# Optimization experiments

Measured on AMD Instinct MI355X. Metric: run time of the kernel, lower is better.

Reference implementation:

```python
import jax, jax.numpy as jnp
import numpy as np

N1, F_IN, E1 = 50000, 128, 1000000   # data1: 10 graphs x 5000 nodes
B, NPG = 10, 5000
N2, E2 = 199, 4000                    # data2: fixed by fc1 in-dim 9950 = 50*199
K = 50
LN_EPS = 1e-5


def setup_inputs() -> dict:
    key = jax.random.key(0)
    ks = jax.random.split(key, 24)
    s = lambda k, shape: (jax.random.normal(k, shape, jnp.float32) * 0.05)
    inp = {}
    inp["x1"] = jax.random.normal(ks[0], (N1, F_IN), jnp.float32)
    inp["edge_index1"] = jax.random.randint(ks[1], (2, E1), 0, N1, jnp.int32)
    inp["batch1"] = jnp.repeat(jnp.arange(B, dtype=jnp.int32), NPG)  # equal-size graphs
    inp["x2"] = jax.random.normal(ks[2], (N2, F_IN), jnp.float32)
    inp["edge_index2"] = jax.random.randint(ks[3], (2, E2), 0, N2, jnp.int32)
    # GNN params (shared Siamese weights). PyG SAGEConv: lin_l (aggr, has bias), lin_r (root, no bias)
    inp["w1l"] = s(ks[4], (128, F_IN)); inp["b1l"] = jnp.zeros((128,), jnp.float32)
    inp["w1r"] = s(ks[5], (128, F_IN))
    inp["w2l"] = s(ks[6], (64, 128));   inp["b2l"] = jnp.zeros((64,), jnp.float32)
    inp["w2r"] = s(ks[7], (64, 128))
    # MLP head
    inp["fc1_w"] = s(ks[8], (128, K * N2)); inp["fc1_b"] = jnp.zeros((128,), jnp.float32)
    inp["ln1_g"] = jnp.ones((128,), jnp.float32); inp["ln1_b"] = jnp.zeros((128,), jnp.float32)
    inp["fc2_w"] = s(ks[9], (64, 128)); inp["fc2_b"] = jnp.zeros((64,), jnp.float32)
    inp["ln2_g"] = jnp.ones((64,), jnp.float32); inp["ln2_b"] = jnp.zeros((64,), jnp.float32)
    inp["fc3_w"] = s(ks[10], (1, 64)); inp["fc3_b"] = jnp.zeros((1,), jnp.float32)
    return inp


def _sage(x, edge_index, wl, bl, wr, n_nodes):
    # mean aggregation of source features at target nodes, then two linears
    src, dst = edge_index[0], edge_index[1]
    msg_sum = jax.ops.segment_sum(x[src], dst, num_segments=n_nodes)
    cnt = jax.ops.segment_sum(jnp.ones((edge_index.shape[1], 1), x.dtype), dst,
                              num_segments=n_nodes)
    mean = msg_sum / jnp.maximum(cnt, 1.0)
    return mean @ wl.T + bl + x @ wr.T


def _gnn(x, ei, w1l, b1l, w1r, w2l, b2l, w2r):
    n = x.shape[0]
    h = jax.nn.relu(_sage(x, ei, w1l, b1l, w1r, n))
    return jax.nn.relu(_sage(h, ei, w2l, b2l, w2r, n))


def _layernorm(x, g, b):
    mu = jnp.mean(x, -1, keepdims=True)
    var = jnp.mean((x - mu) ** 2, -1, keepdims=True)
    return (x - mu) * jax.lax.rsqrt(var + LN_EPS) * g + b


def reference(x1, edge_index1, batch1, x2, edge_index2,
              w1l, b1l, w1r, w2l, b2l, w2r,
              fc1_w, fc1_b, ln1_g, ln1_b, fc2_w, fc2_b, ln2_g, ln2_b, fc3_w, fc3_b):
    out1 = _gnn(x1, edge_index1, w1l, b1l, w1r, w2l, b2l, w2r)   # [N1, 64]
    out2 = _gnn(x2, edge_index2, w1l, b1l, w1r, w2l, b2l, w2r)   # [N2, 64]
    # cdist p=2
    a2 = jnp.sum(out1 * out1, -1, keepdims=True)                 # [N1,1]
    b2 = jnp.sum(out2 * out2, -1)                                # [N2]
    d2 = a2 + b2[None, :] - 2.0 * (out1 @ out2.T)
    dist = jnp.sqrt(jnp.maximum(d2, 0.0))                        # [N1, N2]
    # SortAggregation(k=50): per-graph sort rows by last column (desc), take top k.
    # batch1 groups equal-size graphs contiguously -> reshape is exact dense batching.
    xb = dist.reshape(B, NPG, N2)
    order = jnp.argsort(-xb[:, :, -1], axis=1)[:, :K]            # [B, K]
    topk = jnp.take_along_axis(xb, order[:, :, None], axis=1)    # [B, K, N2]
    out = topk.reshape(B, K * N2)
    out = jax.nn.relu(_layernorm(out @ fc1_w.T + fc1_b, ln1_g, ln1_b))
    out = jax.nn.relu(_layernorm(out @ fc2_w.T + fc2_b, ln2_g, ln2_b))
    out = jax.nn.sigmoid(out @ fc3_w.T + fc3_b)                  # [B, 1]
    return out
```

## Files before the change

kernel.cpp:

```cpp
#include <hip/hip_runtime.h>
#include <math.h>

#define N1 50000
#define F_IN 128
#define E1 1000000
#define Bg 10
#define NPG 5000
#define N2 199
#define E2 4000
#define KSEL 50
#define LN_EPS 1e-5f
#define CHUNKS 8
#define CHSZ 625
#define EBT 8192
#define NB 49
#define BCAP 24576

typedef unsigned long long ull;

__global__ void k_bucket(const int* __restrict__ ei1, int* __restrict__ bcnt,
                         unsigned int* __restrict__ bed,
                         const int* __restrict__ ei2, int* __restrict__ rp2,
                         int* __restrict__ srcs2) {
  int t = threadIdx.x;
  int blk = blockIdx.x;
  const int nEdgeBlocks = (E1 + EBT - 1) / EBT;
  if (blk == nEdgeBlocks) {
    __shared__ int cnt2[N2];
    __shared__ int cur2[N2];
    const int* src = ei2;
    const int* dst = ei2 + E2;
    for (int i = t; i < N2; i += 256) cnt2[i] = 0;
    __syncthreads();
    for (int e = t; e < E2; e += 256) atomicAdd(&cnt2[dst[e]], 1);
    __syncthreads();
    if (t == 0) {
      int run = 0;
      rp2[0] = 0;
      for (int i = 0; i < N2; i++) {
        cur2[i] = run;
        run += cnt2[i];
        rp2[i + 1] = run;
      }
    }
    __syncthreads();
    for (int e = t; e < E2; e += 256) {
      int d = dst[e];
      int pos = atomicAdd(&cur2[d], 1);
      srcs2[pos] = src[e];
    }
    return;
  }
  __shared__ int hcnt[NB];
  const int* src = ei1;
  const int* dst = ei1 + E1;
  int e0 = blk * EBT;
  int e1 = min(e0 + EBT, E1);
  if (t < NB) hcnt[t] = 0;
  __syncthreads();
  for (int e = e0 + t; e < e1; e += 256) atomicAdd(&hcnt[dst[e] >> 10], 1);
  __syncthreads();
  if (t < NB) hcnt[t] = atomicAdd(&bcnt[t], hcnt[t]);
  __syncthreads();
  for (int e = e0 + t; e < e1; e += 256) {
    int d = dst[e];
    int s = src[e];
    int b = d >> 10;
    int pos = atomicAdd(&hcnt[b], 1);
    if (pos < BCAP)
      bed[(size_t)b * BCAP + pos] = ((unsigned int)(d & 1023) << 16) | (unsigned int)s;
  }
}

__global__ __launch_bounds__(1024) void k_csr_bucket(
    const int* __restrict__ bcnt, const unsigned int* __restrict__ bed,
    int* __restrict__ rp, int* __restrict__ srcs) {
  __shared__ int cnt[1024];
  __shared__ int cur[1024];
  __shared__ int wsums[16];
  __shared__ int s_bbase;
  int b = blockIdx.x, t = threadIdx.x;
  int lane = t & 63, w = t >> 6;
  int total = bcnt[b];
  if (total > BCAP) total = BCAP;
  cnt[t] = 0;
  if (w == 0) {
    int vb = (lane < b) ? min(bcnt[lane], BCAP) : 0;
    for (int off = 32; off; off >>= 1) vb += __shfl_xor(vb, off);
    if (lane == 0) s_bbase = vb;
  }
  __syncthreads();
  const unsigned int* list = bed + (size_t)b * BCAP;
  for (int e = t; e < total; e += 1024) atomicAdd(&cnt[list[e] >> 16], 1);
  __syncthreads();
  int v = cnt[t];
  int x = v;
#pragma unroll
  for (int off = 1; off < 64; off <<= 1) {
    int y = __shfl_up(x, off);
    if (lane >= off) x += y;
  }
  if (lane == 63) wsums[w] = x;
  __syncthreads();
  if (w == 0) {
    int s = (lane < 16) ? wsums[lane] : 0;
#pragma unroll
    for (int off = 1; off < 16; off <<= 1) {
      int y = __shfl_up(s, off);
      if (lane >= off) s += y;
    }
    if (lane < 16) wsums[lane] = s;
  }
  __syncthreads();
  int incl = x + (w > 0 ? wsums[w - 1] : 0);
  int bbase = s_bbase;
  int node = b * 1024 + t;
  if (node < N1) rp[node + 1] = bbase + incl;
  cur[t] = bbase + incl - v;
  if (b == 0 && t == 0) rp[0] = 0;
  __syncthreads();
  for (int e = t; e < total; e += 1024) {
    unsigned int pe = list[e];
    int dl = pe >> 16;
    int pos = atomicAdd(&cur[dl], 1);
    srcs[pos] = (int)(pe & 0xFFFFu);
  }
}

__global__ void k_aggr128(const float* __restrict__ xA, const int* __restrict__ rpA,
                          const int* __restrict__ srcsA, float* __restrict__ meanA, int nA,
                          const float* __restrict__ xB, const int* __restrict__ rpB,
                          const int* __restrict__ srcsB, float* __restrict__ meanB, int nB,
                          int blocksA) {
  int blk = blockIdx.x;
  const float* x;
  const int* rp;
  const int* srcs;
  float* mean;
  int n, nb0;
  if (blk < blocksA) { x = xA; rp = rpA; srcs = srcsA; mean = meanA; n = nA; nb0 = blk * 4; }
  else { x = xB; rp = rpB; srcs = srcsB; mean = meanB; n = nB; nb0 = (blk - blocksA) * 4; }
  int lane = threadIdx.x & 63;
  int node = nb0 + (threadIdx.x >> 6);
  if (node >= n) return;
  int s = rp[node], e = rp[node + 1];
  const float2* xp = (const float2*)x;
  float2 acc = make_float2(0.f, 0.f);
  int i = s;
  for (; i + 8 <= e; i += 8) {
    int s0 = srcs[i], s1 = srcs[i + 1], s2 = srcs[i + 2], s3 = srcs[i + 3];
    int s4 = srcs[i + 4], s5 = srcs[i + 5], s6 = srcs[i + 6], s7 = srcs[i + 7];
    float2 v0 = xp[(size_t)s0 * 64 + lane];
    float2 v1 = xp[(size_t)s1 * 64 + lane];
    float2 v2 = xp[(size_t)s2 * 64 + lane];
    float2 v3 = xp[(size_t)s3 * 64 + lane];
    float2 v4 = xp[(size_t)s4 * 64 + lane];
    float2 v5 = xp[(size_t)s5 * 64 + lane];
    float2 v6 = xp[(size_t)s6 * 64 + lane];
    float2 v7 = xp[(size_t)s7 * 64 + lane];
    acc.x += ((v0.x + v1.x) + (v2.x + v3.x)) + ((v4.x + v5.x) + (v6.x + v7.x));
    acc.y += ((v0.y + v1.y) + (v2.y + v3.y)) + ((v4.y + v5.y) + (v6.y + v7.y));
  }
  for (; i < e; i++) {
    float2 v = xp[(size_t)srcs[i] * 64 + lane];
    acc.x += v.x;
    acc.y += v.y;
  }
  float c = (float)((e - s) > 0 ? (e - s) : 1);
  float2 o = make_float2(acc.x / c, acc.y / c);
  *(float2*)&mean[(size_t)node * 128 + lane * 2] = o;
}

__global__ void k_aggr_fused64(const float* __restrict__ zA, const int* __restrict__ rpA,
                               const int* __restrict__ srcsA, float* __restrict__ outA, int nA,
                               const float* __restrict__ zB, const int* __restrict__ rpB,
                               const int* __restrict__ srcsB, float* __restrict__ outB, int nB,
                               const float* __restrict__ bias, int blocksA) {
  int blk = blockIdx.x;
  const float* zlr;
  const int* rp;
  const int* srcs;
  float* out;
  int n, nb0;
  if (blk < blocksA) { zlr = zA; rp = rpA; srcs = srcsA; out = outA; n = nA; nb0 = blk * 4; }
  else { zlr = zB; rp = rpB; srcs = srcsB; out = outB; n = nB; nb0 = (blk - blocksA) * 4; }
  int lane = threadIdx.x & 63;
  int node = nb0 + (threadIdx.x >> 6);
  if (node >= n) return;
  int s = rp[node], e = rp[node + 1];
  float acc = 0.f;
  int i = s;
  for (; i + 8 <= e; i += 8) {
    int s0 = srcs[i], s1 = srcs[i + 1], s2 = srcs[i + 2], s3 = srcs[i + 3];
    int s4 = srcs[i + 4], s5 = srcs[i + 5], s6 = srcs[i + 6], s7 = srcs[i + 7];
    float v0 = zlr[(size_t)s0 * 128 + lane];
    float v1 = zlr[(size_t)s1 * 128 + lane];
    float v2 = zlr[(size_t)s2 * 128 + lane];
    float v3 = zlr[(size_t)s3 * 128 + lane];
    float v4 = zlr[(size_t)s4 * 128 + lane];
    float v5 = zlr[(size_t)s5 * 128 + lane];
    float v6 = zlr[(size_t)s6 * 128 + lane];
    float v7 = zlr[(size_t)s7 * 128 + lane];
    acc += ((v0 + v1) + (v2 + v3)) + ((v4 + v5) + (v6 + v7));
  }
  for (; i < e; i++) acc += zlr[(size_t)srcs[i] * 128 + lane];
  float c = (float)((e - s) > 0 ? (e - s) : 1);
  float v = acc / c + bias[lane] + zlr[(size_t)node * 128 + 64 + lane];
  out[(size_t)node * 64 + lane] = v > 0.f ? v : 0.f;
}

__global__ __launch_bounds__(256) void k_sage_gemm128(
    const float* __restrict__ xinA, const float* __restrict__ meanA,
    float* __restrict__ outA, int nA,
    const float* __restrict__ xinB, const float* __restrict__ meanB,
    float* __restrict__ outB, int nB,
    const float* __restrict__ wl, const float* __restrict__ bl,
    const float* __restrict__ wr, int blocksA) {
  constexpr int TM = 128, TK = 32;
  constexpr int SA = TM + 4;
  constexpr int SW = 128 + 4;
  __shared__ float s_a[TK][SA];
  __shared__ float s_w[TK][SW];
  int blk = blockIdx.x;
  const float* xin;
  const float* mean;
  float* out;
  int n, m0;
  if (blk < blocksA) { xin = xinA; mean = meanA; out = outA; n = nA; m0 = blk * TM; }
  else { xin = xinB; mean = meanB; out = outB; n = nB; m0 = (blk - blocksA) * TM; }
  int t = threadIdx.x;
  int tx = t & 15, ty = t >> 4;
  int sub = t >> 3;
  int kv = (t & 7) << 2;

  float acc[8][8];
#pragma unroll
  for (int i = 0; i < 8; i++)
#pragma unroll
    for (int j = 0; j < 8; j++) acc[i][j] = 0.f;

  for (int ph = 0; ph < 2; ph++) {
    const float* A = ph ? xin : mean;
    const float* W = ph ? wr : wl;
    for (int k0 = 0; k0 < 128; k0 += TK) {
      __syncthreads();
#pragma unroll
      for (int p = 0; p < 4; p++) {
        int node = m0 + p * 32 + sub;
        float4 v = make_float4(0.f, 0.f, 0.f, 0.f);
        if (node < n) v = *(const float4*)&A[(size_t)node * 128 + k0 + kv];
        int col = p * 32 + sub;
        s_a[kv + 0][col] = v.x;
        s_a[kv + 1][col] = v.y;
        s_a[kv + 2][col] = v.z;
        s_a[kv + 3][col] = v.w;
      }
#pragma unroll
      for (int p = 0; p < 4; p++) {
        int j = p * 32 + sub;
        float4 v = *(const float4*)&W[(size_t)j * 128 + k0 + kv];
        s_w[kv + 0][j] = v.x;
        s_w[kv + 1][j] = v.y;
        s_w[kv + 2][j] = v.z;
        s_w[kv + 3][j] = v.w;
      }
      __syncthreads();
#pragma unroll 8
      for (int kk = 0; kk < TK; kk++) {
        float4 a0 = *(const float4*)&s_a[kk][ty * 8];
        float4 a1 = *(const float4*)&s_a[kk][ty * 8 + 4];
        float av[8] = {a0.x, a0.y, a0.z, a0.w, a1.x, a1.y, a1.z, a1.w};
        float4 w0 = *(const float4*)&s_w[kk][tx * 8];
        float4 w1 = *(const float4*)&s_w[kk][tx * 8 + 4];
        float wv[8] = {w0.x, w0.y, w0.z, w0.w, w1.x, w1.y, w1.z, w1.w};
#pragma unroll
        for (int i = 0; i < 8; i++)
#pragma unroll
          for (int j = 0; j < 8; j++) acc[i][j] = fmaf(av[i], wv[j], acc[i][j]);
      }
    }
  }
  float bj[8];
#pragma unroll
  for (int j = 0; j < 8; j++) bj[j] = bl[tx * 8 + j];
#pragma unroll
  for (int i = 0; i < 8; i++) {
    int node = m0 + ty * 8 + i;
    if (node < n) {
#pragma unroll
      for (int q = 0; q < 8; q += 4) {
        float v0 = acc[i][q + 0] + bj[q + 0];
        float v1 = acc[i][q + 1] + bj[q + 1];
        float v2 = acc[i][q + 2] + bj[q + 2];
        float v3 = acc[i][q + 3] + bj[q + 3];
        float4 o;
        o.x = v0 > 0.f ? v0 : 0.f;
        o.y = v1 > 0.f ? v1 : 0.f;
        o.z = v2 > 0.f ? v2 : 0.f;
        o.w = v3 > 0.f ? v3 : 0.f;
        *(float4*)&out[(size_t)node * 128 + tx * 8 + q] = o;
      }
    }
  }
}

__global__ __launch_bounds__(256) void k_lin_dual(
    const float* __restrict__ AA, float* __restrict__ zA, int nA,
    const float* __restrict__ AB, float* __restrict__ zB, int nB,
    const float* __restrict__ wl, const float* __restrict__ wr, int blocksA) {
  constexpr int TM = 128, TK = 32;
  constexpr int SA = TM + 4;
  constexpr int SW = 128 + 4;
  __shared__ float s_a[TK][SA];
  __shared__ float s_w[TK][SW];
  int blk = blockIdx.x;
  const float* A;
  float* zlr;
  int n, m0;
  if (blk < blocksA) { A = AA; zlr = zA; n = nA; m0 = blk * TM; }
  else { A = AB; zlr = zB; n = nB; m0 = (blk - blocksA) * TM; }
  int t = threadIdx.x;
  int tx = t & 15, ty = t >> 4;
  int sub = t >> 3;
  int kv = (t & 7) << 2;

  float acc[8][8];
#pragma unroll
  for (int i = 0; i < 8; i++)
#pragma unroll
    for (int j = 0; j < 8; j++) acc[i][j] = 0.f;

  for (int k0 = 0; k0 < 128; k0 += TK) {
    __syncthreads();
#pragma unroll
    for (int p = 0; p < 4; p++) {
      int node = m0 + p * 32 + sub;
      float4 v = make_float4(0.f, 0.f, 0.f, 0.f);
      if (node < n) v = *(const float4*)&A[(size_t)node * 128 + k0 + kv];
      int col = p * 32 + sub;
      s_a[kv + 0][col] = v.x;
      s_a[kv + 1][col] = v.y;
      s_a[kv + 2][col] = v.z;
      s_a[kv + 3][col] = v.w;
    }
#pragma unroll
    for (int p = 0; p < 4; p++) {
      int j = p * 32 + sub;
      const float* W = (j < 64) ? &wl[(size_t)j * 128] : &wr[(size_t)(j - 64) * 128];
      float4 v = *(const float4*)&W[k0 + kv];
      s_w[kv + 0][j] = v.x;
      s_w[kv + 1][j] = v.y;
      s_w[kv + 2][j] = v.z;
      s_w[kv + 3][j] = v.w;
    }
    __syncthreads();
#pragma unroll 8
    for (int kk = 0; kk < TK; kk++) {
      float4 a0 = *(const float4*)&s_a[kk][ty * 8];
      float4 a1 = *(const float4*)&s_a[kk][ty * 8 + 4];
      float av[8] = {a0.x, a0.y, a0.z, a0.w, a1.x, a1.y, a1.z, a1.w};
      float4 w0 = *(const float4*)&s_w[kk][tx * 8];
      float4 w1 = *(const float4*)&s_w[kk][tx * 8 + 4];
      float wv[8] = {w0.x, w0.y, w0.z, w0.w, w1.x, w1.y, w1.z, w1.w};
#pragma unroll
      for (int i = 0; i < 8; i++)
#pragma unroll
        for (int j = 0; j < 8; j++) acc[i][j] = fmaf(av[i], wv[j], acc[i][j]);
    }
  }
#pragma unroll
  for (int i = 0; i < 8; i++) {
    int node = m0 + ty * 8 + i;
    if (node < n) {
#pragma unroll
      for (int q = 0; q < 8; q += 4) {
        float4 o = make_float4(acc[i][q + 0], acc[i][q + 1], acc[i][q + 2], acc[i][q + 3]);
        *(float4*)&zlr[(size_t)node * 128 + tx * 8 + q] = o;
      }
    }
  }
}

__global__ void k_score_topk_local(const float* __restrict__ out1,
                                   const float* __restrict__ out2,
                                   ull* __restrict__ cand) {
  __shared__ ull s[1024];
  __shared__ float brow[64];
  int blk = blockIdx.x;
  int b = blk >> 3, c = blk & 7;
  int t = threadIdx.x;
  if (t < 64) brow[t] = out2[198 * 64 + t];
  __syncthreads();
  const float4* b4 = (const float4*)brow;
  float b2 = 0.f;
#pragma unroll
  for (int q = 0; q < 16; q++) {
    float4 w = b4[q];
    b2 = fmaf(w.x, w.x, fmaf(w.y, w.y, fmaf(w.z, w.z, fmaf(w.w, w.w, b2))));
  }
#pragma unroll
  for (int p = 0; p < 4; p++) {
    int i = p * 256 + t;
    ull key = 0ULL;
    if (i < CHSZ) {
      int gidx = c * CHSZ + i;
      const float4* ap = (const float4*)&out1[((size_t)b * NPG + gidx) * 64];
      float dot = 0.f, a2 = 0.f;
#pragma unroll
      for (int q = 0; q < 16; q++) {
        float4 a = ap[q];
        float4 w = b4[q];
        dot = fmaf(a.x, w.x, fmaf(a.y, w.y, fmaf(a.z, w.z, fmaf(a.w, w.w, dot))));
        a2 = fmaf(a.x, a.x, fmaf(a.y, a.y, fmaf(a.z, a.z, fmaf(a.w, a.w, a2))));
      }
      float d2 = a2 + b2 - 2.f * dot;
      float sc = sqrtf(fmaxf(d2, 0.f));
      key = ((ull)__float_as_uint(sc) << 32) | (unsigned int)(~gidx);
    }
    s[i] = key;
  }
  __syncthreads();
  for (int k = 2; k <= 1024; k <<= 1) {
    for (int j = k >> 1; j > 0; j >>= 1) {
#pragma unroll
      for (int p = 0; p < 4; p++) {
        int i = p * 256 + t;
        int l = i ^ j;
        if (l > i) {
          bool up = ((i & k) != 0);
          ull a = s[i], bb = s[l];
          if ((a > bb) == up) { s[i] = bb; s[l] = a; }
        }
      }
      __syncthreads();
    }
  }
  if (t < KSEL) cand[(b * CHUNKS + c) * KSEL + t] = s[t];
}

__global__ void k_topk_merge(const ull* __restrict__ cand, int* __restrict__ sel) {
  __shared__ ull s[512];
  int b = blockIdx.x, t = threadIdx.x;
#pragma unroll
  for (int p = 0; p < 2; p++) {
    int i = p * 256 + t;
    s[i] = (i < CHUNKS * KSEL) ? cand[b * CHUNKS * KSEL + i] : 0ULL;
  }
  __syncthreads();
  for (int k = 2; k <= 512; k <<= 1) {
    for (int j = k >> 1; j > 0; j >>= 1) {
#pragma unroll
      for (int p = 0; p < 2; p++) {
        int i = p * 256 + t;
        int l = i ^ j;
        if (l > i) {
          bool up = ((i & k) != 0);
          ull a = s[i], bb = s[l];
          if ((a > bb) == up) { s[i] = bb; s[l] = a; }
        }
      }
      __syncthreads();
    }
  }
  if (t < KSEL) {
    int gidx = (int)(~((unsigned int)s[t]));
    sel[b * KSEL + t] = b * NPG + gidx;
  }
}

__global__ void k_dist_rows(const float* __restrict__ out1, const float* __restrict__ out2,
                            const int* __restrict__ sel, float* __restrict__ D) {
  __shared__ float arow[64];
  int i = blockIdx.x;
  int t = threadIdx.x;
  int node = sel[i];
  if (t < 64) arow[t] = out1[(size_t)node * 64 + t];
  __syncthreads();
  float a2 = 0.f;
#pragma unroll
  for (int f = 0; f < 64; f++) a2 = fmaf(arow[f], arow[f], a2);
  for (int nn = t; nn < N2; nn += 256) {
    float dot = 0.f, b2 = 0.f;
#pragma unroll 8
    for (int f = 0; f < 64; f++) {
      float bv = out2[nn * 64 + f];
      dot = fmaf(arow[f], bv, dot);
      b2 = fmaf(bv, bv, b2);
    }
    float d2 = a2 + b2 - 2.f * dot;
    D[i * N2 + nn] = sqrtf(fmaxf(d2, 0.f));
  }
}

__global__ void k_fc1_dot(const float* __restrict__ D, const float* __restrict__ w,
                          float* __restrict__ h1pre) {
  constexpr int M = KSEL * N2;
  constexpr int M2 = M / 2;
  int b = blockIdx.x >> 7;
  int j = blockIdx.x & 127;
  int t = threadIdx.x;
  const float2* wp = (const float2*)(w + (size_t)j * M);
  const float2* dp = (const float2*)(D + (size_t)b * M);
  float acc = 0.f;
  for (int m = t; m < M2; m += 256) {
    float2 wv = wp[m];
    float2 dv = dp[m];
    acc = fmaf(dv.x, wv.x, acc);
    acc = fmaf(dv.y, wv.y, acc);
  }
  for (int off = 32; off; off >>= 1) acc += __shfl_xor(acc, off);
  __shared__ float ws_[4];
  int lane = t & 63, wv_ = t >> 6;
  if (lane == 0) ws_[wv_] = acc;
  __syncthreads();
  if (t == 0) h1pre[b * 128 + j] = ws_[0] + ws_[1] + ws_[2] + ws_[3];
}

__global__ void k_fc123(const float* __restrict__ h1pre, const float* __restrict__ fc1b,
                        const float* __restrict__ g1, const float* __restrict__ be1,
                        const float* __restrict__ w2, const float* __restrict__ b2v,
                        const float* __restrict__ g2, const float* __restrict__ be2,
                        const float* __restrict__ w3, const float* __restrict__ b3,
                        float* __restrict__ out) {
  __shared__ float wsum[2];
  __shared__ float sh[128];
  int b = blockIdx.x, t = threadIdx.x;
  float acc = h1pre[b * 128 + t] + fc1b[t];
  int lane = t & 63, wv_ = t >> 6;
  float ssum = acc;
  for (int off = 32; off; off >>= 1) ssum += __shfl_xor(ssum, off);
  if (lane == 0) wsum[wv_] = ssum;
  __syncthreads();
  float mu = (wsum[0] + wsum[1]) / 128.f;
  __syncthreads();
  float d = acc - mu;
  float vv = d * d;
  for (int off = 32; off; off >>= 1) vv += __shfl_xor(vv, off);
  if (lane == 0) wsum[wv_] = vv;
  __syncthreads();
  float var = (wsum[0] + wsum[1]) / 128.f;
  float r = rsqrtf(var + LN_EPS);
  float h = d * r * g1[t] + be1[t];
  sh[t] = h > 0.f ? h : 0.f;
  __syncthreads();
  if (t < 64) {
    float a2 = b2v[t];
#pragma unroll 8
    for (int k = 0; k < 128; k++) a2 = fmaf(sh[k], w2[t * 128 + k], a2);
    float s2 = a2;
    for (int off = 32; off; off >>= 1) s2 += __shfl_xor(s2, off);
    float mu2 = s2 * (1.f / 64.f);
    float d2 = a2 - mu2;
    float vv2 = d2 * d2;
    for (int off = 32; off; off >>= 1) vv2 += __shfl_xor(vv2, off);
    float r2 = rsqrtf(vv2 * (1.f / 64.f) + LN_EPS);
    float h2 = d2 * r2 * g2[t] + be2[t];
    h2 = h2 > 0.f ? h2 : 0.f;
    float pp = h2 * w3[t];
    for (int off = 32; off; off >>= 1) pp += __shfl_xor(pp, off);
    if (t == 0) out[b] = 1.f / (1.f + expf(-(pp + b3[0])));
  }
}

extern "C" void kernel_launch(void* const* d_in, const int* in_sizes, int n_in,
                              void* d_out, int out_size, void* d_ws, size_t ws_size,
                              hipStream_t stream) {
  const float* x1 = (const float*)d_in[0];
  const int* ei1 = (const int*)d_in[1];
  const float* x2 = (const float*)d_in[3];
  const int* ei2 = (const int*)d_in[4];
  const float* w1l = (const float*)d_in[5];
  const float* b1l = (const float*)d_in[6];
  const float* w1r = (const float*)d_in[7];
  const float* w2l = (const float*)d_in[8];
  const float* b2l = (const float*)d_in[9];
  const float* w2r = (const float*)d_in[10];
  const float* fc1w = (const float*)d_in[11];
  const float* fc1b = (const float*)d_in[12];
  const float* ln1g = (const float*)d_in[13];
  const float* ln1b = (const float*)d_in[14];
  const float* fc2w = (const float*)d_in[15];
  const float* fc2b = (const float*)d_in[16];
  const float* ln2g = (const float*)d_in[17];
  const float* ln2b = (const float*)d_in[18];
  const float* fc3w = (const float*)d_in[19];
  const float* fc3b = (const float*)d_in[20];
  float* out = (float*)d_out;

  char* p = (char*)d_ws;
  auto alloc = [&](size_t bytes) {
    char* r = p;
    p += (bytes + 255) & ~(size_t)255;
    return r;
  };
  int* rp1 = (int*)alloc((N1 + 1) * 4);
  int* bcnt = (int*)alloc(NB * 4);
  unsigned int* bed = (unsigned int*)alloc((size_t)NB * BCAP * 4);
  int* srcs1 = (int*)alloc((size_t)E1 * 4);
  int* rp2 = (int*)alloc((N2 + 1) * 4);
  int* srcs2 = (int*)alloc(E2 * 4);
  float* bufMean = (float*)alloc((size_t)N1 * 128 * 4);
  float* bufH = (float*)alloc((size_t)N1 * 128 * 4);
  float* out1b = (float*)alloc((size_t)N1 * 64 * 4);
  float* mean2 = (float*)alloc((size_t)N2 * 128 * 4);
  float* h2g = (float*)alloc((size_t)N2 * 128 * 4);
  float* out2b = (float*)alloc((size_t)N2 * 64 * 4);
  int* sel = (int*)alloc(Bg * KSEL * 4);
  ull* cand = (ull*)alloc((size_t)Bg * CHUNKS * KSEL * 8);
  float* Dm = (float*)alloc((size_t)Bg * KSEL * N2 * 4);
  float* h1pre = (float*)alloc(Bg * 128 * 4);

  const int nEdgeBlocks = (E1 + EBT - 1) / EBT;
  const int aggrBlocksA = (N1 + 3) / 4;
  const int aggrBlocksB = (N2 + 3) / 4;
  const int gemmBlocksA = (N1 + 127) / 128;
  const int gemmBlocksB = (N2 + 127) / 128;

  hipMemsetAsync(bcnt, 0, NB * 4, stream);
  k_bucket<<<nEdgeBlocks + 1, 256, 0, stream>>>(ei1, bcnt, bed, ei2, rp2, srcs2);
  k_csr_bucket<<<NB, 1024, 0, stream>>>(bcnt, bed, rp1, srcs1);
  k_aggr128<<<aggrBlocksA + aggrBlocksB, 256, 0, stream>>>(
      x1, rp1, srcs1, bufMean, N1, x2, rp2, srcs2, mean2, N2, aggrBlocksA);
  k_sage_gemm128<<<gemmBlocksA + gemmBlocksB, 256, 0, stream>>>(
      x1, bufMean, bufH, N1, x2, mean2, h2g, N2, w1l, b1l, w1r, gemmBlocksA);
  k_lin_dual<<<gemmBlocksA + gemmBlocksB, 256, 0, stream>>>(
      bufH, bufMean, N1, h2g, mean2, N2, w2l, w2r, gemmBlocksA);
  k_aggr_fused64<<<aggrBlocksA + aggrBlocksB, 256, 0, stream>>>(
      bufMean, rp1, srcs1, out1b, N1, mean2, rp2, srcs2, out2b, N2, b2l, aggrBlocksA);
  k_score_topk_local<<<Bg * CHUNKS, 256, 0, stream>>>(out1b, out2b, cand);
  k_topk_merge<<<Bg, 256, 0, stream>>>(cand, sel);
  k_dist_rows<<<Bg * KSEL, 256, 0, stream>>>(out1b, out2b, sel, Dm);
  k_fc1_dot<<<Bg * 128, 256, 0, stream>>>(Dm, fc1w, h1pre);
  k_fc123<<<Bg, 128, 0, stream>>>(h1pre, fc1b, ln1g, ln1b, fc2w, fc2b, ln2g, ln2b,
                                  fc3w, fc3b, out);
}
```

Measured before the change: 415.0 us.

## Fuse SAGE layer-1 and layer-2 GEMMs, merge topk with dist, batch fc1

Merges the layer-1 SAGE GEMM and the layer-2 dual linear into one kernel with 64-row tiles. The intermediate hidden activations stay in shared memory (transposed) instead of round-tripping through a global buffer. It also fuses the top-k merge with the distance-row computation, dropping one launch and the sel buffer. The fc1 dot is restructured so each block handles one output column for all 10 graphs, so fc1 weights are read once instead of ten times. The trade-offs are larger shared memory per block, smaller M-tiles, fewer blocks in the merge/dist and fc1 stages, and an in-place overwrite of bufMean that depends on each block reading only its own rows.

```diff
diff --git a/kernel.cpp b/kernel.cpp
--- a/kernel.cpp
+++ b/kernel.cpp
@@ -209,173 +209,127 @@
   out[(size_t)node * 64 + lane] = v > 0.f ? v : 0.f;
 }
 
-__global__ __launch_bounds__(256) void k_sage_gemm128(
-    const float* __restrict__ xinA, const float* __restrict__ meanA,
-    float* __restrict__ outA, int nA,
-    const float* __restrict__ xinB, const float* __restrict__ meanB,
-    float* __restrict__ outB, int nB,
-    const float* __restrict__ wl, const float* __restrict__ bl,
-    const float* __restrict__ wr, int blocksA) {
-  constexpr int TM = 128, TK = 32;
-  constexpr int SA = TM + 4;
-  constexpr int SW = 128 + 4;
-  __shared__ float s_a[TK][SA];
-  __shared__ float s_w[TK][SW];
+__global__ __launch_bounds__(256) void k_sage12(
+    const float* __restrict__ xinA, float* __restrict__ zA, int nA,
+    const float* __restrict__ xinB, float* __restrict__ zB, int nB,
+    const float* __restrict__ w1l, const float* __restrict__ b1l,
+    const float* __restrict__ w1r, const float* __restrict__ w2l,
+    const float* __restrict__ w2r, int blocksA) {
+  constexpr int TM = 64, TK = 32;
+  __shared__ float s_a[TK][TM + 4];
+  __shared__ float s_w[TK][132];
+  __shared__ float s_hT[128][TM + 4];
   int blk = blockIdx.x;
   const float* xin;
-  const float* mean;
-  float* out;
+  float* zlr;
   int n, m0;
-  if (blk < blocksA) { xin = xinA; mean = meanA; out = outA; n = nA; m0 = blk * TM; }
-  else { xin = xinB; mean = meanB; out = outB; n = nB; m0 = (blk - blocksA) * TM; }
+  if (blk < blocksA) { xin = xinA; zlr = zA; n = nA; m0 = blk * TM; }
+  else { xin = xinB; zlr = zB; n = nB; m0 = (blk - blocksA) * TM; }
   int t = threadIdx.x;
   int tx = t & 15, ty = t >> 4;
-  int sub = t >> 3;
-  int kv = (t & 7) << 2;
-
-  float acc[8][8];
-#pragma unroll
-  for (int i = 0; i < 8; i++)
+
+  float acc[4][8];
+#pragma unroll
+  for (int i = 0; i < 4; i++)
 #pragma unroll
     for (int j = 0; j < 8; j++) acc[i][j] = 0.f;
 
   for (int ph = 0; ph < 2; ph++) {
-    const float* A = ph ? xin : mean;
-    const float* W = ph ? wr : wl;
+    const float* A = ph ? xin : zlr;
+    const float* W = ph ? w1r : w1l;
     for (int k0 = 0; k0 < 128; k0 += TK) {
       __syncthreads();
 #pragma unroll
+      for (int p = 0; p < 2; p++) {
+        int idx = p * 256 + t;
+        int nl = idx >> 3, kq = (idx & 7) << 2;
+        int gn = m0 + nl;
+        float4 v = make_float4(0.f, 0.f, 0.f, 0.f);
+        if (gn < n) v = *(const float4*)&A[(size_t)gn * 128 + k0 + kq];
+        s_a[kq + 0][nl] = v.x;
+        s_a[kq + 1][nl] = v.y;
+        s_a[kq + 2][nl] = v.z;
+        s_a[kq + 3][nl] = v.w;
+      }
+#pragma unroll
       for (int p = 0; p < 4; p++) {
-        int node = m0 + p * 32 + sub;
-        float4 v = make_float4(0.f, 0.f, 0.f, 0.f);
-        if (node < n) v = *(const float4*)&A[(size_t)node * 128 + k0 + kv];
-        int col = p * 32 + sub;
-        s_a[kv + 0][col] = v.x;
-        s_a[kv + 1][col] = v.y;
-        s_a[kv + 2][col] = v.z;
-        s_a[kv + 3][col] = v.w;
-      }
-#pragma unroll
-      for (int p = 0; p < 4; p++) {
-        int j = p * 32 + sub;
-        float4 v = *(const float4*)&W[(size_t)j * 128 + k0 + kv];
-        s_w[kv + 0][j] = v.x;
-        s_w[kv + 1][j] = v.y;
-        s_w[kv + 2][j] = v.z;
-        s_w[kv + 3][j] = v.w;
+        int idx = p * 256 + t;
+        int j = idx >> 3, kq = (idx & 7) << 2;
+        float4 v = *(const float4*)&W[(size_t)j * 128 + k0 + kq];
+        s_w[kq + 0][j] = v.x;
+        s_w[kq + 1][j] = v.y;
+        s_w[kq + 2][j] = v.z;
+        s_w[kq + 3][j] = v.w;
       }
       __syncthreads();
 #pragma unroll 8
       for (int kk = 0; kk < TK; kk++) {
-        float4 a0 = *(const float4*)&s_a[kk][ty * 8];
-        float4 a1 = *(const float4*)&s_a[kk][ty * 8 + 4];
-        float av[8] = {a0.x, a0.y, a0.z, a0.w, a1.x, a1.y, a1.z, a1.w};
+        float4 a0 = *(const float4*)&s_a[kk][ty * 4];
+        float av[4] = {a0.x, a0.y, a0.z, a0.w};
         float4 w0 = *(const float4*)&s_w[kk][tx * 8];
         float4 w1 = *(const float4*)&s_w[kk][tx * 8 + 4];
         float wv[8] = {w0.x, w0.y, w0.z, w0.w, w1.x, w1.y, w1.z, w1.w};
 #pragma unroll
-        for (int i = 0; i < 8; i++)
+        for (int i = 0; i < 4; i++)
 #pragma unroll
           for (int j = 0; j < 8; j++) acc[i][j] = fmaf(av[i], wv[j], acc[i][j]);
       }
     }
   }
-  float bj[8];
-#pragma unroll
-  for (int j = 0; j < 8; j++) bj[j] = bl[tx * 8 + j];
-#pragma unroll
-  for (int i = 0; i < 8; i++) {
-    int node = m0 + ty * 8 + i;
-    if (node < n) {
-#pragma unroll
-      for (int q = 0; q < 8; q += 4) {
-        float v0 = acc[i][q + 0] + bj[q + 0];
-        float v1 = acc[i][q + 1] + bj[q + 1];
-        float v2 = acc[i][q + 2] + bj[q + 2];
-        float v3 = acc[i][q + 3] + bj[q + 3];
-        float4 o;
-        o.x = v0 > 0.f ? v0 : 0.f;
-        o.y = v1 > 0.f ? v1 : 0.f;
-        o.z = v2 > 0.f ? v2 : 0.f;
-        o.w = v3 > 0.f ? v3 : 0.f;
-        *(float4*)&out[(size_t)node * 128 + tx * 8 + q] = o;
-      }
-    }
-  }
-}
-
-__global__ __launch_bounds__(256) void k_lin_dual(
-    const float* __restrict__ AA, float* __restrict__ zA, int nA,
-    const float* __restrict__ AB, float* __restrict__ zB, int nB,
-    const float* __restrict__ wl, const float* __restrict__ wr, int blocksA) {
-  constexpr int TM = 128, TK = 32;
-  constexpr int SA = TM + 4;
-  constexpr int SW = 128 + 4;
-  __shared__ float s_a[TK][SA];
-  __shared__ float s_w[TK][SW];
-  int blk = blockIdx.x;
-  const float* A;
-  float* zlr;
-  int n, m0;
-  if (blk < blocksA) { A = AA; zlr = zA; n = nA; m0 = blk * TM; }
-  else { A = AB; zlr = zB; n = nB; m0 = (blk - blocksA) * TM; }
-  int t = threadIdx.x;
-  int tx = t & 15, ty = t >> 4;
-  int sub = t >> 3;
-  int kv = (t & 7) << 2;
-
-  float acc[8][8];
-#pragma unroll
-  for (int i = 0; i < 8; i++)
-#pragma unroll
-    for (int j = 0; j < 8; j++) acc[i][j] = 0.f;
-
+  __syncthreads();
+#pragma unroll
+  for (int q = 0; q < 8; q++) {
+    int j = tx * 8 + q;
+    float b = b1l[j];
+    float4 hv;
+    float h0 = acc[0][q] + b, h1 = acc[1][q] + b, h2 = acc[2][q] + b, h3 = acc[3][q] + b;
+    hv.x = h0 > 0.f ? h0 : 0.f;
+    hv.y = h1 > 0.f ? h1 : 0.f;
+    hv.z = h2 > 0.f ? h2 : 0.f;
+    hv.w = h3 > 0.f ? h3 : 0.f;
+    *(float4*)&s_hT[j][ty * 4] = hv;
+  }
+
+  float acc2[4][8];
+#pragma unroll
+  for (int i = 0; i < 4; i++)
+#pragma unroll
+    for (int j = 0; j < 8; j++) acc2[i][j] = 0.f;
   for (int k0 = 0; k0 < 128; k0 += TK) {
     __syncthreads();
 #pragma unroll
     for (int p = 0; p < 4; p++) {
-      int node = m0 + p * 32 + sub;
-      float4 v = make_float4(0.f, 0.f, 0.f, 0.f);
-      if (node < n) v = *(const float4*)&A[(size_t)node * 128 + k0 + kv];
-      int col = p * 32 + sub;
-      s_a[kv + 0][col] = v.x;
-      s_a[kv + 1][col] = v.y;
-      s_a[kv + 2][col] = v.z;
-      s_a[kv + 3][col] = v.w;
-    }
-#pragma unroll
-    for (int p = 0; p < 4; p++) {
-      int j = p * 32 + sub;
-      const float* W = (j < 64) ? &wl[(size_t)j * 128] : &wr[(size_t)(j - 64) * 128];
-      float4 v = *(const float4*)&W[k0 + kv];
-      s_w[kv + 0][j] = v.x;
-      s_w[kv + 1][j] = v.y;
-      s_w[kv + 2][j] = v.z;
-      s_w[kv + 3][j] = v.w;
+      int idx = p * 256 + t;
+      int j = idx >> 3, kq = (idx & 7) << 2;
+      const float* W2 = (j < 64) ? &w2l[(size_t)j * 128] : &w2r[(size_t)(j - 64) * 128];
+      float4 v = *(const float4*)&W2[k0 + kq];
+      s_w[kq + 0][j] = v.x;
+      s_w[kq + 1][j] = v.y;
+      s_w[kq + 2][j] = v.z;
+      s_w[kq + 3][j] = v.w;
     }
     __syncthreads();
 #pragma unroll 8
     for (int kk = 0; kk < TK; kk++) {
-      float4 a0 = *(const float4*)&s_a[kk][ty * 8];
-      float4 a1 = *(const float4*)&s_a[kk][ty * 8 + 4];
-      float av[8] = {a0.x, a0.y, a0.z, a0.w, a1.x, a1.y, a1.z, a1.w};
+      float4 a0 = *(const float4*)&s_hT[k0 + kk][ty * 4];
+      float av[4] = {a0.x, a0.y, a0.z, a0.w};
       float4 w0 = *(const float4*)&s_w[kk][tx * 8];
       float4 w1 = *(const float4*)&s_w[kk][tx * 8 + 4];
       float wv[8] = {w0.x, w0.y, w0.z, w0.w, w1.x, w1.y, w1.z, w1.w};
 #pragma unroll
-      for (int i = 0; i < 8; i++)
-#pragma unroll
-        for (int j = 0; j < 8; j++) acc[i][j] = fmaf(av[i], wv[j], acc[i][j]);
-    }
-  }
-#pragma unroll
-  for (int i = 0; i < 8; i++) {
-    int node = m0 + ty * 8 + i;
-    if (node < n) {
+      for (int i = 0; i < 4; i++)
+#pragma unroll
+        for (int j = 0; j < 8; j++) acc2[i][j] = fmaf(av[i], wv[j], acc2[i][j]);
+    }
+  }
+#pragma unroll
+  for (int i = 0; i < 4; i++) {
+    int gn = m0 + ty * 4 + i;
+    if (gn < n) {
 #pragma unroll
       for (int q = 0; q < 8; q += 4) {
-        float4 o = make_float4(acc[i][q + 0], acc[i][q + 1], acc[i][q + 2], acc[i][q + 3]);
-        *(float4*)&zlr[(size_t)node * 128 + tx * 8 + q] = o;
+        float4 o = make_float4(acc2[i][q + 0], acc2[i][q + 1], acc2[i][q + 2], acc2[i][q + 3]);
+        *(float4*)&zlr[(size_t)gn * 128 + tx * 8 + q] = o;
       }
     }
   }
@@ -438,8 +392,12 @@
   if (t < KSEL) cand[(b * CHUNKS + c) * KSEL + t] = s[t];
 }
 
-__global__ void k_topk_merge(const ull* __restrict__ cand, int* __restrict__ sel) {
+__global__ void k_merge_dist(const ull* __restrict__ cand, const float* __restrict__ out1,
+                             const float* __restrict__ out2, float* __restrict__ D) {
   __shared__ ull s[512];
+  __shared__ float s_a[KSEL][64];
+  __shared__ float s_a2[KSEL];
+  __shared__ int s_nd[KSEL];
   int b = blockIdx.x, t = threadIdx.x;
 #pragma unroll
   for (int p = 0; p < 2; p++) {
@@ -464,31 +422,40 @@
   }
   if (t < KSEL) {
     int gidx = (int)(~((unsigned int)s[t]));
-    sel[b * KSEL + t] = b * NPG + gidx;
-  }
-}
-
-__global__ void k_dist_rows(const float* __restrict__ out1, const float* __restrict__ out2,
-                            const int* __restrict__ sel, float* __restrict__ D) {
-  __shared__ float arow[64];
-  int i = blockIdx.x;
-  int t = threadIdx.x;
-  int node = sel[i];
-  if (t < 64) arow[t] = out1[(size_t)node * 64 + t];
-  __syncthreads();
-  float a2 = 0.f;
-#pragma unroll
-  for (int f = 0; f < 64; f++) a2 = fmaf(arow[f], arow[f], a2);
-  for (int nn = t; nn < N2; nn += 256) {
+    s_nd[t] = b * NPG + gidx;
+  }
+  __syncthreads();
+  for (int idx = t; idx < KSEL * 64; idx += 256) {
+    int i = idx >> 6, f = idx & 63;
+    s_a[i][f] = out1[(size_t)s_nd[i] * 64 + f];
+  }
+  __syncthreads();
+  if (t < KSEL) {
+    float a2 = 0.f;
+    const float4* ap = (const float4*)&s_a[t][0];
+#pragma unroll
+    for (int q = 0; q < 16; q++) {
+      float4 a = ap[q];
+      a2 = fmaf(a.x, a.x, fmaf(a.y, a.y, fmaf(a.z, a.z, fmaf(a.w, a.w, a2))));
+    }
+    s_a2[t] = a2;
+  }
+  __syncthreads();
+  for (int widx = t; widx < KSEL * N2; widx += 256) {
+    int i = widx / N2;
+    int nn = widx - i * N2;
+    const float4* ap = (const float4*)&s_a[i][0];
+    const float4* bp = (const float4*)&out2[(size_t)nn * 64];
     float dot = 0.f, b2 = 0.f;
-#pragma unroll 8
-    for (int f = 0; f < 64; f++) {
-      float bv = out2[nn * 64 + f];
-      dot = fmaf(arow[f], bv, dot);
-      b2 = fmaf(bv, bv, b2);
-    }
-    float d2 = a2 + b2 - 2.f * dot;
-    D[i * N2 + nn] = sqrtf(fmaxf(d2, 0.f));
+#pragma unroll
+    for (int q = 0; q < 16; q++) {
+      float4 a = ap[q];
+      float4 w = bp[q];
+      dot = fmaf(a.x, w.x, fmaf(a.y, w.y, fmaf(a.z, w.z, fmaf(a.w, w.w, dot))));
+      b2 = fmaf(w.x, w.x, fmaf(w.y, w.y, fmaf(w.z, w.z, fmaf(w.w, w.w, b2))));
+    }
+    float d2 = s_a2[i] + b2 - 2.f * dot;
+    D[(size_t)b * KSEL * N2 + widx] = sqrtf(fmaxf(d2, 0.f));
   }
 }
 
@@ -496,24 +463,30 @@
                           float* __restrict__ h1pre) {
   constexpr int M = KSEL * N2;
   constexpr int M2 = M / 2;
-  int b = blockIdx.x >> 7;
-  int j = blockIdx.x & 127;
+  int j = blockIdx.x;
   int t = threadIdx.x;
   const float2* wp = (const float2*)(w + (size_t)j * M);
-  const float2* dp = (const float2*)(D + (size_t)b * M);
-  float acc = 0.f;
+  float acc[Bg];
+#pragma unroll
+  for (int b = 0; b < Bg; b++) acc[b] = 0.f;
   for (int m = t; m < M2; m += 256) {
     float2 wv = wp[m];
-    float2 dv = dp[m];
-    acc = fmaf(dv.x, wv.x, acc);
-    acc = fmaf(dv.y, wv.y, acc);
-  }
-  for (int off = 32; off; off >>= 1) acc += __shfl_xor(acc, off);
-  __shared__ float ws_[4];
+#pragma unroll
+    for (int b = 0; b < Bg; b++) {
+      float2 dv = ((const float2*)(D + (size_t)b * M))[m];
+      acc[b] = fmaf(dv.x, wv.x, fmaf(dv.y, wv.y, acc[b]));
+    }
+  }
+  __shared__ float ws_[4][Bg];
   int lane = t & 63, wv_ = t >> 6;
-  if (lane == 0) ws_[wv_] = acc;
-  __syncthreads();
-  if (t == 0) h1pre[b * 128 + j] = ws_[0] + ws_[1] + ws_[2] + ws_[3];
+#pragma unroll
+  for (int b = 0; b < Bg; b++) {
+    float v = acc[b];
+    for (int off = 32; off; off >>= 1) v += __shfl_xor(v, off);
+    if (lane == 0) ws_[wv_][b] = v;
+  }
+  __syncthreads();
+  if (t < Bg) h1pre[t * 128 + j] = ws_[0][t] + ws_[1][t] + ws_[2][t] + ws_[3][t];
 }
 
 __global__ void k_fc123(const float* __restrict__ h1pre, const float* __restrict__ fc1b,
@@ -600,12 +573,9 @@
   int* rp2 = (int*)alloc((N2 + 1) * 4);
   int* srcs2 = (int*)alloc(E2 * 4);
   float* bufMean = (float*)alloc((size_t)N1 * 128 * 4);
-  float* bufH = (float*)alloc((size_t)N1 * 128 * 4);
   float* out1b = (float*)alloc((size_t)N1 * 64 * 4);
   float* mean2 = (float*)alloc((size_t)N2 * 128 * 4);
-  float* h2g = (float*)alloc((size_t)N2 * 128 * 4);
   float* out2b = (float*)alloc((size_t)N2 * 64 * 4);
-  int* sel = (int*)alloc(Bg * KSEL * 4);
   ull* cand = (ull*)alloc((size_t)Bg * CHUNKS * KSEL * 8);
   float* Dm = (float*)alloc((size_t)Bg * KSEL * N2 * 4);
   float* h1pre = (float*)alloc(Bg * 128 * 4);
@@ -613,24 +583,21 @@
   const int nEdgeBlocks = (E1 + EBT - 1) / EBT;
   const int aggrBlocksA = (N1 + 3) / 4;
   const int aggrBlocksB = (N2 + 3) / 4;
-  const int gemmBlocksA = (N1 + 127) / 128;
-  const int gemmBlocksB = (N2 + 127) / 128;
+  const int sageBlocksA = (N1 + 63) / 64;
+  const int sageBlocksB = (N2 + 63) / 64;
 
   hipMemsetAsync(bcnt, 0, NB * 4, stream);
   k_bucket<<<nEdgeBlocks + 1, 256, 0, stream>>>(ei1, bcnt, bed, ei2, rp2, srcs2);
   k_csr_bucket<<<NB, 1024, 0, stream>>>(bcnt, bed, rp1, srcs1);
   k_aggr128<<<aggrBlocksA + aggrBlocksB, 256, 0, stream>>>(
       x1, rp1, srcs1, bufMean, N1, x2, rp2, srcs2, mean2, N2, aggrBlocksA);
-  k_sage_gemm128<<<gemmBlocksA + gemmBlocksB, 256, 0, stream>>>(
-      x1, bufMean, bufH, N1, x2, mean2, h2g, N2, w1l, b1l, w1r, gemmBlocksA);
-  k_lin_dual<<<gemmBlocksA + gemmBlocksB, 256, 0, stream>>>(
-      bufH, bufMean, N1, h2g, mean2, N2, w2l, w2r, gemmBlocksA);
+  k_sage12<<<sageBlocksA + sageBlocksB, 256, 0, stream>>>(
+      x1, bufMean, N1, x2, mean2, N2, w1l, b1l, w1r, w2l, w2r, sageBlocksA);
   k_aggr_fused64<<<aggrBlocksA + aggrBlocksB, 256, 0, stream>>>(
       bufMean, rp1, srcs1, out1b, N1, mean2, rp2, srcs2, out2b, N2, b2l, aggrBlocksA);
   k_score_topk_local<<<Bg * CHUNKS, 256, 0, stream>>>(out1b, out2b, cand);
-  k_topk_merge<<<Bg, 256, 0, stream>>>(cand, sel);
-  k_dist_rows<<<Bg * KSEL, 256, 0, stream>>>(out1b, out2b, sel, Dm);
-  k_fc1_dot<<<Bg * 128, 256, 0, stream>>>(Dm, fc1w, h1pre);
+  k_merge_dist<<<Bg, 256, 0, stream>>>(cand, out1b, out2b, Dm);
+  k_fc1_dot<<<128, 256, 0, stream>>>(Dm, fc1w, h1pre);
   k_fc123<<<Bg, 128, 0, stream>>>(h1pre, fc1b, ln1g, ln1b, fc2w, fc2b, ln2g, ln2b,
                                   fc3w, fc3b, out);
 }
```

Measured after the change: 498.0 us. 20.0% more time.

## Fuse top-k merge with distance rows and batch fc1 across graphs

Applied to the files above, without the earlier changes.

Merges the top-k merge kernel with the selected-row distance computation, so each of the 10 blocks sorts its candidates, loads the 50 selected rows into shared memory and computes their distances to all 199 out2 rows with float4 loads. This removes one launch and the intermediate sel buffer. The fc1 dot kernel now launches one block per output neuron and accumulates all 10 graphs in registers, so each fc1 weight row (about 5 MB total) is read once instead of ten times. The cost is lower parallelism: only 10 blocks for the distance stage and 128 blocks for fc1.

```diff
diff --git a/kernel.cpp b/kernel.cpp
--- a/kernel.cpp
+++ b/kernel.cpp
@@ -438,8 +438,12 @@
   if (t < KSEL) cand[(b * CHUNKS + c) * KSEL + t] = s[t];
 }
 
-__global__ void k_topk_merge(const ull* __restrict__ cand, int* __restrict__ sel) {
+__global__ void k_merge_dist(const ull* __restrict__ cand, const float* __restrict__ out1,
+                             const float* __restrict__ out2, float* __restrict__ D) {
   __shared__ ull s[512];
+  __shared__ float s_a[KSEL][64];
+  __shared__ float s_a2[KSEL];
+  __shared__ int s_nd[KSEL];
   int b = blockIdx.x, t = threadIdx.x;
 #pragma unroll
   for (int p = 0; p < 2; p++) {
@@ -464,31 +468,40 @@
   }
   if (t < KSEL) {
     int gidx = (int)(~((unsigned int)s[t]));
-    sel[b * KSEL + t] = b * NPG + gidx;
-  }
-}
-
-__global__ void k_dist_rows(const float* __restrict__ out1, const float* __restrict__ out2,
-                            const int* __restrict__ sel, float* __restrict__ D) {
-  __shared__ float arow[64];
-  int i = blockIdx.x;
-  int t = threadIdx.x;
-  int node = sel[i];
-  if (t < 64) arow[t] = out1[(size_t)node * 64 + t];
-  __syncthreads();
-  float a2 = 0.f;
-#pragma unroll
-  for (int f = 0; f < 64; f++) a2 = fmaf(arow[f], arow[f], a2);
-  for (int nn = t; nn < N2; nn += 256) {
+    s_nd[t] = b * NPG + gidx;
+  }
+  __syncthreads();
+  for (int idx = t; idx < KSEL * 64; idx += 256) {
+    int i = idx >> 6, f = idx & 63;
+    s_a[i][f] = out1[(size_t)s_nd[i] * 64 + f];
+  }
+  __syncthreads();
+  if (t < KSEL) {
+    float a2 = 0.f;
+    const float4* ap = (const float4*)&s_a[t][0];
+#pragma unroll
+    for (int q = 0; q < 16; q++) {
+      float4 a = ap[q];
+      a2 = fmaf(a.x, a.x, fmaf(a.y, a.y, fmaf(a.z, a.z, fmaf(a.w, a.w, a2))));
+    }
+    s_a2[t] = a2;
+  }
+  __syncthreads();
+  for (int widx = t; widx < KSEL * N2; widx += 256) {
+    int i = widx / N2;
+    int nn = widx - i * N2;
+    const float4* ap = (const float4*)&s_a[i][0];
+    const float4* bp = (const float4*)&out2[(size_t)nn * 64];
     float dot = 0.f, b2 = 0.f;
-#pragma unroll 8
-    for (int f = 0; f < 64; f++) {
-      float bv = out2[nn * 64 + f];
-      dot = fmaf(arow[f], bv, dot);
-      b2 = fmaf(bv, bv, b2);
-    }
-    float d2 = a2 + b2 - 2.f * dot;
-    D[i * N2 + nn] = sqrtf(fmaxf(d2, 0.f));
+#pragma unroll
+    for (int q = 0; q < 16; q++) {
+      float4 a = ap[q];
+      float4 w = bp[q];
+      dot = fmaf(a.x, w.x, fmaf(a.y, w.y, fmaf(a.z, w.z, fmaf(a.w, w.w, dot))));
+      b2 = fmaf(w.x, w.x, fmaf(w.y, w.y, fmaf(w.z, w.z, fmaf(w.w, w.w, b2))));
+    }
+    float d2 = s_a2[i] + b2 - 2.f * dot;
+    D[(size_t)b * KSEL * N2 + widx] = sqrtf(fmaxf(d2, 0.f));
   }
 }
 
@@ -496,24 +509,30 @@
                           float* __restrict__ h1pre) {
   constexpr int M = KSEL * N2;
   constexpr int M2 = M / 2;
-  int b = blockIdx.x >> 7;
-  int j = blockIdx.x & 127;
+  int j = blockIdx.x;
   int t = threadIdx.x;
   const float2* wp = (const float2*)(w + (size_t)j * M);
-  const float2* dp = (const float2*)(D + (size_t)b * M);
-  float acc = 0.f;
+  float acc[Bg];
+#pragma unroll
+  for (int b = 0; b < Bg; b++) acc[b] = 0.f;
   for (int m = t; m < M2; m += 256) {
     float2 wv = wp[m];
-    float2 dv = dp[m];
-    acc = fmaf(dv.x, wv.x, acc);
-    acc = fmaf(dv.y, wv.y, acc);
-  }
-  for (int off = 32; off; off >>= 1) acc += __shfl_xor(acc, off);
-  __shared__ float ws_[4];
+#pragma unroll
+    for (int b = 0; b < Bg; b++) {
+      float2 dv = ((const float2*)(D + (size_t)b * M))[m];
+      acc[b] = fmaf(dv.x, wv.x, fmaf(dv.y, wv.y, acc[b]));
+    }
+  }
+  __shared__ float ws_[4][Bg];
   int lane = t & 63, wv_ = t >> 6;
-  if (lane == 0) ws_[wv_] = acc;
-  __syncthreads();
-  if (t == 0) h1pre[b * 128 + j] = ws_[0] + ws_[1] + ws_[2] + ws_[3];
+#pragma unroll
+  for (int b = 0; b < Bg; b++) {
+    float v = acc[b];
+    for (int off = 32; off; off >>= 1) v += __shfl_xor(v, off);
+    if (lane == 0) ws_[wv_][b] = v;
+  }
+  __syncthreads();
+  if (t < Bg) h1pre[t * 128 + j] = ws_[0][t] + ws_[1][t] + ws_[2][t] + ws_[3][t];
 }
 
 __global__ void k_fc123(const float* __restrict__ h1pre, const float* __restrict__ fc1b,
@@ -605,7 +624,6 @@
   float* mean2 = (float*)alloc((size_t)N2 * 128 * 4);
   float* h2g = (float*)alloc((size_t)N2 * 128 * 4);
   float* out2b = (float*)alloc((size_t)N2 * 64 * 4);
-  int* sel = (int*)alloc(Bg * KSEL * 4);
   ull* cand = (ull*)alloc((size_t)Bg * CHUNKS * KSEL * 8);
   float* Dm = (float*)alloc((size_t)Bg * KSEL * N2 * 4);
   float* h1pre = (float*)alloc(Bg * 128 * 4);
@@ -628,9 +646,8 @@
   k_aggr_fused64<<<aggrBlocksA + aggrBlocksB, 256, 0, stream>>>(
       bufMean, rp1, srcs1, out1b, N1, mean2, rp2, srcs2, out2b, N2, b2l, aggrBlocksA);
   k_score_topk_local<<<Bg * CHUNKS, 256, 0, stream>>>(out1b, out2b, cand);
-  k_topk_merge<<<Bg, 256, 0, stream>>>(cand, sel);
-  k_dist_rows<<<Bg * KSEL, 256, 0, stream>>>(out1b, out2b, sel, Dm);
-  k_fc1_dot<<<Bg * 128, 256, 0, stream>>>(Dm, fc1w, h1pre);
+  k_merge_dist<<<Bg, 256, 0, stream>>>(cand, out1b, out2b, Dm);
+  k_fc1_dot<<<128, 256, 0, stream>>>(Dm, fc1w, h1pre);
   k_fc123<<<Bg, 128, 0, stream>>>(h1pre, fc1b, ln1g, ln1b, fc2w, fc2b, ln2g, ln2b,
                                   fc3w, fc3b, out);
 }
```

New measurement: 485.4 us. 1.17x slower.
